# Performance work log

Measured on AMD Instinct MI355X. Metric: run time of the kernel, lower is better.

The kernel has to match this reference:

```python
import jax, jax.numpy as jnp
import numpy as np

EMB_DIM = 2048
USER_DIM = 256
NUM_EXPERTS = 64
TOP_K = 8
N_TOKENS = 16384


def setup_inputs() -> dict:
    key = jax.random.key(0)
    k_h, k_u, k_w = jax.random.split(key, 3)
    h = jax.random.normal(k_h, (N_TOKENS, EMB_DIM), dtype=jnp.float32)
    u = jax.random.normal(k_u, (N_TOKENS, USER_DIM), dtype=jnp.float32)
    # nn.Linear weight is [out, in]; we store transposed [in, out] for x @ W
    W = jax.random.normal(k_w, (EMB_DIM + USER_DIM, NUM_EXPERTS), dtype=jnp.float32) * (1.0 / np.sqrt(EMB_DIM + USER_DIM))
    b = jnp.zeros((NUM_EXPERTS,), dtype=jnp.float32)
    return {"h": h, "u": u, "W": W, "b": b}


def reference(h, u, W, b):
    # gate logits: [N, E]
    g = jnp.concatenate([h, u], axis=-1) @ W + b
    w = jax.nn.softmax(g, axis=-1)
    # top-k mask + renormalize (top_k < num_experts)
    _, top_idx = jax.lax.top_k(w, TOP_K)                       # [N, k]
    mask = jax.nn.one_hot(top_idx, NUM_EXPERTS, dtype=w.dtype).sum(axis=-2)  # [N, E]
    w = w * mask
    w = w / (w.sum(axis=-1, keepdims=True) + 1e-9)
    return w
```

## Files before the change

kernel.cpp:

```cpp
#include <hip/hip_runtime.h>

#define EMB 2048
#define UDIM 256
#define KTOT 2304
#define NE 64
#define TOPK 8
#define SSH 6144
#define STEPB 12288
#define KSPL 12
#define SPS 6
#define SLICEB (SPS * STEPB)
#define NB 64
#define NTOK 16384
#define PART_OFF (1 << 20)

typedef __attribute__((ext_vector_type(8))) short short8;
typedef __attribute__((ext_vector_type(4))) float f32x4;
typedef __attribute__((ext_vector_type(4))) unsigned int u32x4;

__device__ __forceinline__ unsigned short bf16h(float x) {
  unsigned uu = __builtin_bit_cast(unsigned, x);
  return (unsigned short)((uu + 0x7FFFu + ((uu >> 16) & 1u)) >> 16);
}
__device__ __forceinline__ float bf2f(unsigned short s) {
  return __builtin_bit_cast(float, ((unsigned)s) << 16);
}

__device__ __forceinline__ unsigned cvtpk(float a, float b) {
  unsigned r;
  asm("v_cvt_pk_bf16_f32 %0, %1, %2" : "=v"(r) : "v"(a), "v"(b));
  return r;
}

__device__ __forceinline__ f32x4 gld(const float* p) {
  f32x4 r;
  asm volatile("global_load_dwordx4 %0, %1, off" : "=v"(r) : "v"(p) : "memory");
  return r;
}

__global__ __launch_bounds__(256)
void prep_w(const float* __restrict__ W, unsigned short* __restrict__ wb) {
  const int flat = blockIdx.x * 256 + threadIdx.x;
  const int k = flat >> 6;
  const int n = flat & 63;
  const float w = W[flat];
  const unsigned short h0 = bf16h(w);
  const float r1 = w - bf2f(h0);
  const unsigned short h1 = bf16h(r1);
  const float r2 = r1 - bf2f(h1);
  const unsigned short h2 = bf16h(r2);

  const int s = k >> 5;
  const int kk = k & 31;
  const int lane = (kk >> 3) * 16 + (n & 15);
  const int j = kk & 7;
  const int nt = n >> 4;
  const size_t base = (size_t)s * SSH + ((size_t)nt * 64 + lane) * 8 + j;
  wb[base] = h0;
  wb[base + 2048] = h1;
  wb[base + 4096] = h2;
}

__device__ __forceinline__ void step_math(const f32x4& c0, const f32x4& c1,
                                          const short8* Bv, f32x4* acc) {
  const float xs[8] = {c0[0], c0[1], c0[2], c0[3],
                       c1[0], c1[1], c1[2], c1[3]};
  u32x4 W0, W1, W2;
#pragma unroll
  for (int k2 = 0; k2 < 4; ++k2) {
    const float a = xs[2 * k2], bbv = xs[2 * k2 + 1];
    const unsigned p0 = cvtpk(a, bbv);
    const float a1 = a - __builtin_bit_cast(float, p0 << 16);
    const float b1 = bbv - __builtin_bit_cast(float, p0 & 0xFFFF0000u);
    const unsigned p1 = cvtpk(a1, b1);
    const float a2 = a1 - __builtin_bit_cast(float, p1 << 16);
    const float b2 = b1 - __builtin_bit_cast(float, p1 & 0xFFFF0000u);
    const unsigned p2 = cvtpk(a2, b2);
    W0[k2] = p0; W1[k2] = p1; W2[k2] = p2;
  }
  const short8 A0 = __builtin_bit_cast(short8, W0);
  const short8 A1 = __builtin_bit_cast(short8, W1);
  const short8 A2 = __builtin_bit_cast(short8, W2);

#pragma unroll
  for (int nt = 0; nt < 4; ++nt) {
    acc[nt] = __builtin_amdgcn_mfma_f32_16x16x32_bf16(A0, Bv[0 + nt], acc[nt], 0, 0, 0);
    acc[nt] = __builtin_amdgcn_mfma_f32_16x16x32_bf16(A0, Bv[4 + nt], acc[nt], 0, 0, 0);
    acc[nt] = __builtin_amdgcn_mfma_f32_16x16x32_bf16(A1, Bv[0 + nt], acc[nt], 0, 0, 0);
    acc[nt] = __builtin_amdgcn_mfma_f32_16x16x32_bf16(A1, Bv[4 + nt], acc[nt], 0, 0, 0);
    acc[nt] = __builtin_amdgcn_mfma_f32_16x16x32_bf16(A0, Bv[8 + nt], acc[nt], 0, 0, 0);
    acc[nt] = __builtin_amdgcn_mfma_f32_16x16x32_bf16(A2, Bv[0 + nt], acc[nt], 0, 0, 0);
  }
}

#define STEP(S, NW, alo, ahi)                                              \
  do {                                                                     \
    asm volatile("s_waitcnt vmcnt(" #NW ")" : "+v"(alo), "+v"(ahi));       \
    short8 Bv[12];                                                         \
    _Pragma("unroll")                                                      \
    for (int q = 0; q < 12; ++q)                                           \
      Bv[q] = *(const short8*)(lb + (S) * STEPB + q * 1024);               \
    step_math(alo, ahi, Bv, acc);                                          \
  } while (0)

__global__ __launch_bounds__(512, 4)
void gate_split(const float* __restrict__ h, const float* __restrict__ u,
                const unsigned short* __restrict__ wb,
                float* __restrict__ partial) {
  __shared__ __align__(1024) char lds[SLICEB];

  const int tid = threadIdx.x;
  const int lane = tid & 63;
  const int wid = __builtin_amdgcn_readfirstlane(tid >> 6);
  const int kq = blockIdx.x >> 6;
  const int bb = blockIdx.x & 63;
  const int mm = lane & 15;
  const int q8 = (lane >> 4) * 8;

  const char* src = (const char*)wb + (size_t)kq * SLICEB + (size_t)lane * 16;
  for (int j = wid; j < SPS * 12; j += 8)
    __builtin_amdgcn_global_load_lds(
        (const __attribute__((address_space(1))) unsigned int*)(src + (size_t)j * 1024),
        (__attribute__((address_space(3))) unsigned int*)(lds + (size_t)j * 1024),
        16, 0, 0);
  __syncthreads();

  const char* lb = lds + (size_t)lane * 16;
  const int ks0 = kq * SPS;

#pragma unroll 1
  for (int tt = 0; tt < 2; ++tt) {
    const int tile = (bb * 8 + wid) * 2 + tt;
    const int token = tile * 16 + mm;
    const float* hrow = h + (size_t)token * EMB + q8;
    const float* urow = u + (size_t)token * UDIM + q8;

    f32x4 a0l, a0h, a1l, a1h, a2l, a2h, a3l, a3h, a4l, a4h, a5l, a5h;
#define AISSUE(S, vlo, vhi)                                                \
    {                                                                      \
      const int as = ks0 + (S);                                            \
      const float* ps = (as < 64) ? (hrow + as * 32)                       \
                                  : (urow + (as - 64) * 32);               \
      vlo = gld(ps);                                                       \
      vhi = gld(ps + 4);                                                   \
    }
    AISSUE(0, a0l, a0h)
    AISSUE(1, a1l, a1h)
    AISSUE(2, a2l, a2h)
    AISSUE(3, a3l, a3h)
    AISSUE(4, a4l, a4h)
    AISSUE(5, a5l, a5h)
#undef AISSUE

    f32x4 acc[4];
#pragma unroll
    for (int nt = 0; nt < 4; ++nt) acc[nt] = 0.f;

    STEP(0, 10, a0l, a0h);
    STEP(1, 8, a1l, a1h);
    STEP(2, 6, a2l, a2h);
    STEP(3, 4, a3l, a3h);
    STEP(4, 2, a4l, a4h);
    STEP(5, 0, a5l, a5h);

    const int rowb = (lane >> 4) * 4;
#pragma unroll
    for (int nt = 0; nt < 4; ++nt)
#pragma unroll
      for (int r = 0; r < 4; ++r)
        partial[((size_t)kq * NTOK + tile * 16 + rowb + r) * NE + nt * 16 + mm] =
            acc[nt][r];
  }
}

__global__ __launch_bounds__(256)
void finalize(const float* __restrict__ partial, const float* __restrict__ b,
              float* __restrict__ out) {
  const int tid = threadIdx.x;
  const int lane = tid & 63;
  const int wv = tid >> 6;
  const int t = blockIdx.x * 4 + wv;
  const float bias = b[lane];

  float g = bias;
#pragma unroll
  for (int s = 0; s < KSPL; ++s)
    g += partial[((size_t)s * NTOK + t) * NE + lane];

  float m = g;
#pragma unroll
  for (int off = 32; off > 0; off >>= 1)
    m = fmaxf(m, __shfl_xor(m, off));
  float pexp = __expf(g - m);
  float sum = pexp;
#pragma unroll
  for (int off = 32; off > 0; off >>= 1)
    sum += __shfl_xor(sum, off);
  const float pn = pexp / sum;

  float vv = pn;
  float topsum = 0.f;
  int sel = 0;
  for (int r = 0; r < TOPK; ++r) {
    float mv = vv;
    int mi = lane;
#pragma unroll
    for (int off = 32; off > 0; off >>= 1) {
      const float ov = __shfl_xor(mv, off);
      const int oi = __shfl_xor(mi, off);
      if (ov > mv || (ov == mv && oi < mi)) { mv = ov; mi = oi; }
    }
    topsum += mv;
    if (lane == mi) { sel = 1; vv = -1.f; }
  }

  out[(size_t)t * NE + lane] = sel ? pn / (topsum + 1e-9f) : 0.f;
}

extern "C" void kernel_launch(void* const* d_in, const int* in_sizes, int n_in,
                              void* d_out, int out_size, void* d_ws, size_t ws_size,
                              hipStream_t stream) {
  const float* h = (const float*)d_in[0];
  const float* u = (const float*)d_in[1];
  const float* W = (const float*)d_in[2];
  const float* b = (const float*)d_in[3];
  float* out = (float*)d_out;

  unsigned short* wb = (unsigned short*)d_ws;
  float* partial = (float*)((char*)d_ws + PART_OFF);

  hipLaunchKernelGGL(prep_w, dim3(KTOT * NE / 256), dim3(256), 0, stream, W, wb);
  hipLaunchKernelGGL(gate_split, dim3(KSPL * NB), dim3(512), 0, stream,
                     h, u, wb, partial);
  hipLaunchKernelGGL(finalize, dim3(NTOK / 4), dim3(256), 0, stream,
                     partial, b, out);
}
```

Measured before the change: 258.6 us.

## Rebalance K-split and double-buffer activation loads across four tiles per wave

The K dimension is now split 8 ways with 9 steps per slice instead of 12 ways with 6, so only one block of 512 threads runs per CU, using a larger LDS-resident weight slice. Each wave now handles four token tiles and software-pipelines them: the next tile's global activation loads are issued into a second register buffer while the current tile is still computing, with vmcnt waits tuned for this. The last slice gets a special address path for the h/u boundary. The aim is to hide global-load latency and to cut partial-sum traffic for the finalize kernel, at the cost of lower occupancy and higher register pressure.

```diff
diff --git a/kernel.cpp b/kernel.cpp
--- a/kernel.cpp
+++ b/kernel.cpp
@@ -7,10 +7,9 @@
 #define TOPK 8
 #define SSH 6144
 #define STEPB 12288
-#define KSPL 12
-#define SPS 6
+#define KSPL 8
+#define SPS 9
 #define SLICEB (SPS * STEPB)
-#define NB 64
 #define NTOK 16384
 #define PART_OFF (1 << 20)
 
@@ -93,17 +92,33 @@
   }
 }
 
-#define STEP(S, NW, alo, ahi)                                              \
+#define TSTEP(S, NW, Arr)                                                  \
   do {                                                                     \
-    asm volatile("s_waitcnt vmcnt(" #NW ")" : "+v"(alo), "+v"(ahi));       \
+    asm volatile("s_waitcnt vmcnt(" #NW ")"                                \
+                 : "+v"(Arr[2 * (S)]), "+v"(Arr[2 * (S) + 1]));            \
     short8 Bv[12];                                                         \
     _Pragma("unroll")                                                      \
     for (int q = 0; q < 12; ++q)                                           \
       Bv[q] = *(const short8*)(lb + (S) * STEPB + q * 1024);               \
-    step_math(alo, ahi, Bv, acc);                                          \
+    step_math(Arr[2 * (S)], Arr[2 * (S) + 1], Bv, acc);                    \
   } while (0)
 
-__global__ __launch_bounds__(512, 4)
+#define AISSUE(tile_, Arr)                                                 \
+  do {                                                                     \
+    const int _tok = (tile_) * 16 + mm;                                    \
+    const float* _hr = h + (size_t)_tok * EMB + q8;                        \
+    const float* _ur = u + (size_t)_tok * UDIM + q8;                       \
+    _Pragma("unroll")                                                      \
+    for (int s = 0; s < SPS; ++s) {                                        \
+      const float* _ps;                                                    \
+      if (!tail) _ps = _hr + (ks0 + s) * 32;                               \
+      else _ps = (s == 0) ? (_hr + 2016) : (_ur + (s - 1) * 32);           \
+      Arr[2 * s] = gld(_ps);                                               \
+      Arr[2 * s + 1] = gld(_ps + 4);                                       \
+    }                                                                      \
+  } while (0)
+
+__global__ __launch_bounds__(512, 1)
 void gate_split(const float* __restrict__ h, const float* __restrict__ u,
                 const unsigned short* __restrict__ wb,
                 float* __restrict__ partial) {
@@ -112,8 +127,8 @@
   const int tid = threadIdx.x;
   const int lane = tid & 63;
   const int wid = __builtin_amdgcn_readfirstlane(tid >> 6);
-  const int kq = blockIdx.x >> 6;
-  const int bb = blockIdx.x & 63;
+  const int kq = blockIdx.x >> 5;
+  const int bb = blockIdx.x & 31;
   const int mm = lane & 15;
   const int q8 = (lane >> 4) * 8;
 
@@ -125,52 +140,52 @@
         16, 0, 0);
   __syncthreads();
 
+  const bool tail = (kq == KSPL - 1);
   const char* lb = lds + (size_t)lane * 16;
   const int ks0 = kq * SPS;
-
-#pragma unroll 1
-  for (int tt = 0; tt < 2; ++tt) {
-    const int tile = (bb * 8 + wid) * 2 + tt;
-    const int token = tile * 16 + mm;
-    const float* hrow = h + (size_t)token * EMB + q8;
-    const float* urow = u + (size_t)token * UDIM + q8;
-
-    f32x4 a0l, a0h, a1l, a1h, a2l, a2h, a3l, a3h, a4l, a4h, a5l, a5h;
-#define AISSUE(S, vlo, vhi)                                                \
-    {                                                                      \
-      const int as = ks0 + (S);                                            \
-      const float* ps = (as < 64) ? (hrow + as * 32)                       \
-                                  : (urow + (as - 64) * 32);               \
-      vlo = gld(ps);                                                       \
-      vhi = gld(ps + 4);                                                   \
-    }
-    AISSUE(0, a0l, a0h)
-    AISSUE(1, a1l, a1h)
-    AISSUE(2, a2l, a2h)
-    AISSUE(3, a3l, a3h)
-    AISSUE(4, a4l, a4h)
-    AISSUE(5, a5l, a5h)
-#undef AISSUE
-
-    f32x4 acc[4];
-#pragma unroll
-    for (int nt = 0; nt < 4; ++nt) acc[nt] = 0.f;
-
-    STEP(0, 10, a0l, a0h);
-    STEP(1, 8, a1l, a1h);
-    STEP(2, 6, a2l, a2h);
-    STEP(3, 4, a3l, a3h);
-    STEP(4, 2, a4l, a4h);
-    STEP(5, 0, a5l, a5h);
-
+  const int tb = (bb * 8 + wid) * 4;
+
+  f32x4 acc[4];
+#pragma unroll
+  for (int nt = 0; nt < 4; ++nt) acc[nt] = 0.f;
+
+  auto store = [&](int tile) {
     const int rowb = (lane >> 4) * 4;
 #pragma unroll
-    for (int nt = 0; nt < 4; ++nt)
+    for (int nt = 0; nt < 4; ++nt) {
 #pragma unroll
       for (int r = 0; r < 4; ++r)
         partial[((size_t)kq * NTOK + tile * 16 + rowb + r) * NE + nt * 16 + mm] =
             acc[nt][r];
-  }
+      acc[nt] = 0.f;
+    }
+  };
+
+  f32x4 Aa[2 * SPS], Ab[2 * SPS];
+
+  AISSUE(tb + 0, Aa);
+  TSTEP(0, 16, Aa); TSTEP(1, 14, Aa); TSTEP(2, 12, Aa);
+  TSTEP(3, 10, Aa); TSTEP(4, 8, Aa);
+  AISSUE(tb + 1, Ab);
+  TSTEP(5, 24, Aa); TSTEP(6, 22, Aa); TSTEP(7, 20, Aa); TSTEP(8, 18, Aa);
+  store(tb + 0);
+
+  TSTEP(0, 32, Ab); TSTEP(1, 30, Ab); TSTEP(2, 28, Ab);
+  TSTEP(3, 26, Ab); TSTEP(4, 24, Ab);
+  AISSUE(tb + 2, Aa);
+  TSTEP(5, 40, Ab); TSTEP(6, 38, Ab); TSTEP(7, 36, Ab); TSTEP(8, 34, Ab);
+  store(tb + 1);
+
+  TSTEP(0, 32, Aa); TSTEP(1, 30, Aa); TSTEP(2, 28, Aa);
+  TSTEP(3, 26, Aa); TSTEP(4, 24, Aa);
+  AISSUE(tb + 3, Ab);
+  TSTEP(5, 40, Aa); TSTEP(6, 38, Aa); TSTEP(7, 36, Aa); TSTEP(8, 34, Aa);
+  store(tb + 2);
+
+  TSTEP(0, 32, Ab); TSTEP(1, 30, Ab); TSTEP(2, 28, Ab);
+  TSTEP(3, 26, Ab); TSTEP(4, 24, Ab);
+  TSTEP(5, 22, Ab); TSTEP(6, 20, Ab); TSTEP(7, 18, Ab); TSTEP(8, 16, Ab);
+  store(tb + 3);
 }
 
 __global__ __launch_bounds__(256)
@@ -230,7 +245,7 @@
   float* partial = (float*)((char*)d_ws + PART_OFF);
 
   hipLaunchKernelGGL(prep_w, dim3(KTOT * NE / 256), dim3(256), 0, stream, W, wb);
-  hipLaunchKernelGGL(gate_split, dim3(KSPL * NB), dim3(512), 0, stream,
+  hipLaunchKernelGGL(gate_split, dim3(KSPL * 32), dim3(512), 0, stream,
                      h, u, wb, partial);
   hipLaunchKernelGGL(finalize, dim3(NTOK / 4), dim3(256), 0, stream,
                      partial, b, out);
```

Result: faster. 241.5 us (-6.6%).
